# Optimization experiments

Measured on AMD Instinct MI355X. Metric: run time of the kernel, lower is better.

## Reference

```python
import jax, jax.numpy as jnp
import numpy as np

T, H, I, E, K = 4096, 2048, 1408, 8, 2  # tokens, hidden, intermediate, experts, top_k


def setup_inputs() -> dict:
    key = jax.random.key(0)
    ks = jax.random.split(key, 6)
    hidden_states = jax.random.normal(ks[0], (T, H), dtype=jnp.float32)
    gate_weight = jax.random.normal(ks[1], (E, H), dtype=jnp.float32) * 0.02  # fp32 gate, per source assert
    w13_weight = jax.random.randint(ks[2], (E, 2 * I, H), -127, 128, dtype=jnp.int8)
    w13_weight_scale = jax.random.uniform(ks[3], (E, 2 * I), dtype=jnp.float32, minval=0.5, maxval=1.5) * 0.005
    w2_weight = jax.random.randint(ks[4], (E, H, I), -127, 128, dtype=jnp.int8)
    w2_weight_scale = jax.random.uniform(ks[5], (E, H), dtype=jnp.float32, minval=0.5, maxval=1.5) * 0.005
    return dict(hidden_states=hidden_states, gate_weight=gate_weight,
                w13_weight=w13_weight, w13_weight_scale=w13_weight_scale,
                w2_weight=w2_weight, w2_weight_scale=w2_weight_scale)


def _dynamic_quant_i8(x):
    # per-token dynamic symmetric int8: scale = max|x|/127 (smooth scales default to ones)
    s = jnp.maximum(jnp.max(jnp.abs(x), axis=-1, keepdims=True) / 127.0, 1e-8)
    q = jnp.clip(jnp.round(x / s), -127.0, 127.0)
    return q, s


def reference(hidden_states, gate_weight, w13_weight, w13_weight_scale, w2_weight, w2_weight_scale):
    # --- gating: fp32 linear + topk softmax (renormalize=True) ---
    logits = hidden_states @ gate_weight.T              # [T, E]
    probs = jax.nn.softmax(logits, axis=-1)
    topv, topi = jax.lax.top_k(probs, K)                # [T, K]
    gates = topv / jnp.sum(topv, axis=-1, keepdims=True)
    # dense routing weights [T, E]: gate value where expert selected, else 0
    route = jnp.zeros((T, E), hidden_states.dtype).at[jnp.arange(T)[:, None], topi].add(gates)

    # --- dynamic per-token int8 quant of routed input (same token value for each of its K copies) ---
    q_in, s_in = _dynamic_quant_i8(hidden_states)       # [T, H], [T, 1]

    # --- grouped w8a8 GEMM (fc1) -> SwiGLU -> requant -> grouped GEMM (fc2) -> weighted combine ---
    def step(acc, xs):
        w13, s13, w2, s2w, r = xs                       # per-expert weights / route column [T]
        h1 = (q_in @ w13.T.astype(jnp.float32)) * s_in * s13[None, :]   # dequant fc1: [T, 2I]
        g, u = h1[:, :I], h1[:, I:]
        act = jax.nn.silu(g) * u                        # SwiGLU
        q_a, s_a = _dynamic_quant_i8(act)
        h2 = (q_a @ w2.T.astype(jnp.float32)) * s_a * s2w[None, :]      # dequant fc2: [T, H]
        return acc + r[:, None] * h2, None

    acc0 = jnp.zeros_like(hidden_states)
    out, _ = jax.lax.scan(step, acc0,
                          (w13_weight, w13_weight_scale, w2_weight, w2_weight_scale, route.T))
    return out
```

## Files before the change

kernel.cpp:

```cpp
#include <hip/hip_runtime.h>
#include <hip/hip_bf16.h>

#define T_TOK 4096
#define H_DIM 2048
#define I_DIM 1408
#define E_NUM 8
#define NI2   (2 * I_DIM)
#define NMB   136

typedef int v4i __attribute__((ext_vector_type(4)));

#define GLD_LDS16(gptr, lptr)                                                        \
  __builtin_amdgcn_global_load_lds(                                                  \
      (const __attribute__((address_space(1))) void*)(gptr),                         \
      (__attribute__((address_space(3))) void*)(lptr), 16, 0, 0)

__global__ __launch_bounds__(256) void pack_tiled(
    const int* __restrict__ w13, const int* __restrict__ w2,
    signed char* __restrict__ qw13t, signed char* __restrict__ qw2t) {
  const int id = blockIdx.x;
  const int* src;
  signed char* dst;
  int R, Kd, nb, kc, e;
  if (id < 8 * 22 * 32) {
    e = id / (22 * 32);
    int r = id % (22 * 32);
    nb = r / 32; kc = r % 32;
    src = w13; dst = qw13t + (size_t)id * 8192; R = NI2; Kd = H_DIM;
  } else {
    int j = id - 8 * 22 * 32;
    e = j / (16 * 22);
    int r = j % (16 * 22);
    nb = r / 22; kc = r % 22;
    src = w2; dst = qw2t + (size_t)j * 8192; R = H_DIM; Kd = I_DIM;
  }
  const int tid = threadIdx.x;
  const int seg = tid & 3;
#pragma unroll
  for (int h = 0; h < 2; h++) {
    int row = h * 64 + (tid >> 2);
    const int4* s4 = (const int4*)(src + ((size_t)(e * R + nb * 128 + row) * Kd + kc * 64 + seg * 16));
    int4 v0 = s4[0], v1 = s4[1], v2 = s4[2], v3 = s4[3];
    union { signed char c[16]; int4 v; } pk;
    pk.c[0] = (signed char)v0.x;  pk.c[1] = (signed char)v0.y;
    pk.c[2] = (signed char)v0.z;  pk.c[3] = (signed char)v0.w;
    pk.c[4] = (signed char)v1.x;  pk.c[5] = (signed char)v1.y;
    pk.c[6] = (signed char)v1.z;  pk.c[7] = (signed char)v1.w;
    pk.c[8] = (signed char)v2.x;  pk.c[9] = (signed char)v2.y;
    pk.c[10] = (signed char)v2.z; pk.c[11] = (signed char)v2.w;
    pk.c[12] = (signed char)v3.x; pk.c[13] = (signed char)v3.y;
    pk.c[14] = (signed char)v3.z; pk.c[15] = (signed char)v3.w;
    *(int4*)(dst + h * 4096 + tid * 16) = pk.v;
  }
}

__global__ __launch_bounds__(256) void gate_route_quant(
    const float* __restrict__ hs, const float* __restrict__ gw,
    signed char* __restrict__ qin, float* __restrict__ s_in,
    int* __restrict__ tope, float* __restrict__ gts) {
  const int t = blockIdx.x;
  const int tid = threadIdx.x;
  const int lane = tid & 63;
  const int wave = tid >> 6;
  const float* row = hs + (size_t)t * H_DIM;

  const float4* r4 = (const float4*)row + tid * 2;
  float4 xa = r4[0], xb = r4[1];
  float x[8] = {xa.x, xa.y, xa.z, xa.w, xb.x, xb.y, xb.z, xb.w};

  double pd[8];
  for (int e = 0; e < 8; e++) pd[e] = 0.0;
  float am = 0.f;
  for (int j = 0; j < 8; j++) {
    float v = x[j];
    am = fmaxf(am, fabsf(v));
    int col = tid * 8 + j;
    for (int e = 0; e < 8; e++)
      pd[e] += (double)v * (double)gw[e * H_DIM + col];
  }
  for (int e = 0; e < 8; e++)
    for (int s = 32; s; s >>= 1) pd[e] += __shfl_down(pd[e], s);
  for (int s = 32; s; s >>= 1) am = fmaxf(am, __shfl_down(am, s));

  __shared__ double sred[4][8];
  __shared__ float sam[4];
  __shared__ float sbc;
  if (lane == 0) {
    for (int e = 0; e < 8; e++) sred[wave][e] = pd[e];
    sam[wave] = am;
  }
  __syncthreads();
  if (tid == 0) {
    float l[8];
    for (int e = 0; e < 8; e++)
      l[e] = (float)(sred[0][e] + sred[1][e] + sred[2][e] + sred[3][e]);
    float amx = fmaxf(fmaxf(sam[0], sam[1]), fmaxf(sam[2], sam[3]));
    float s = fmaxf(amx / 127.0f, 1e-8f);
    s_in[t] = s;
    sbc = s;
    int i1 = 0;
    for (int e = 1; e < 8; e++) if (l[e] > l[i1]) i1 = e;
    int i2 = -1;
    for (int e = 0; e < 8; e++) {
      if (e == i1) continue;
      if (i2 < 0 || l[e] > l[i2]) i2 = e;
    }
    float d = expf(l[i2] - l[i1]);
    tope[2 * t] = i1;     gts[2 * t] = 1.0f / (1.0f + d);
    tope[2 * t + 1] = i2; gts[2 * t + 1] = d / (1.0f + d);
  }
  __syncthreads();
  float s = sbc;
  union { signed char c[8]; unsigned long long u; } pk;
  for (int j = 0; j < 8; j++) {
    float q = rintf(x[j] / s);
    q = fminf(127.f, fmaxf(-127.f, q));
    pk.c[j] = (signed char)q;
  }
  ((unsigned long long*)(qin + (size_t)t * H_DIM))[tid] = pk.u;
}

__global__ __launch_bounds__(256) void build_lists(
    const int* __restrict__ tope, int* __restrict__ tok_list,
    int* __restrict__ epos, int* __restrict__ cnt) {
  const int e = blockIdx.x;
  const int tid = threadIdx.x;
  const int lane = tid & 63;
  const int wave = tid >> 6;
  __shared__ int wsum[4];
  __shared__ int base_s;
  if (tid == 0) base_s = 0;
  __syncthreads();
  for (int t0 = 0; t0 < T_TOK; t0 += 256) {
    int t = t0 + tid;
    int i1 = tope[2 * t], i2 = tope[2 * t + 1];
    int slot = (i1 == e) ? 0 : ((i2 == e) ? 1 : -1);
    unsigned long long m = __ballot(slot >= 0);
    int wpre = __popcll(m & ((1ull << lane) - 1ull));
    if (lane == 0) wsum[wave] = __popcll(m);
    __syncthreads();
    int pre = wpre;
    for (int w = 0; w < wave; w++) pre += wsum[w];
    int total = wsum[0] + wsum[1] + wsum[2] + wsum[3];
    int b = base_s;
    if (slot >= 0) {
      int pos = b + pre;
      tok_list[e * T_TOK + pos] = t;
      epos[2 * t + slot] = (e << 16) | pos;
    }
    __syncthreads();
    if (tid == 0) base_s = b + total;
  }
  __syncthreads();
  if (tid == 0) cnt[e] = base_s;
}

__global__ void calc_off(const int* __restrict__ cnt, int* __restrict__ poff) {
  if (threadIdx.x == 0) {
    int p = 0;
    for (int e = 0; e < E_NUM; e++) {
      poff[e] = p;
      p += ((cnt[e] + 63) >> 6) << 6;
    }
  }
}

__global__ __launch_bounds__(256) void tile_a1(
    const signed char* __restrict__ qin, const int* __restrict__ tok_list,
    const int* __restrict__ cnt, const int* __restrict__ poff,
    signed char* __restrict__ qx1) {
  const int e = blockIdx.y;
  const int ce = cnt[e];
  const int m0 = blockIdx.x * 64;
  if (m0 >= ce) return;
  const int pmb = (poff[e] >> 6) + blockIdx.x;
  const int tid = threadIdx.x;
  const int row = tid >> 2, seg = tid & 3;
  const int tok = tok_list[e * T_TOK + min(m0 + row, ce - 1)];
  const signed char* src = qin + (size_t)tok * H_DIM + seg * 16;
  signed char* dstb = qx1 + (size_t)pmb * (32 * 4096) + tid * 16;
#pragma unroll
  for (int kc = 0; kc < 32; kc++)
    *(int4*)(dstb + kc * 4096) = *(const int4*)(src + kc * 64);
}

__global__ __launch_bounds__(256, 3) void gemm1_silu(
    const signed char* __restrict__ qw13t, const signed char* __restrict__ qx1,
    const float* __restrict__ s_in, const float* __restrict__ s13,
    const int* __restrict__ tok_list, const int* __restrict__ cnt,
    const int* __restrict__ poff, __hip_bfloat16* __restrict__ act,
    unsigned int* __restrict__ amax) {
  const int xcd = blockIdx.x & 7;
  const int r = blockIdx.x >> 3;
  const int sl = r >> 6;
  const int mb = r & 63;
  const int s = xcd + 8 * sl;
  const int e = s / 11;
  const int nb = s % 11;

  const int ce = cnt[e];
  const int m0 = mb * 64;
  if (m0 >= ce) return;
  const int n0 = nb * 128;
  const int pmb = (poff[e] >> 6) + mb;

  __shared__ __align__(16) signed char As[4096];
  __shared__ __align__(16) signed char Bg[8192];
  __shared__ __align__(16) signed char Bu[8192];

  const int tid = threadIdx.x;
  const int lane = tid & 63;
  const int wave = tid >> 6;
  const int quad = lane >> 4;
  const int ln = lane & 15;

  const signed char* Ab = qx1 + (size_t)pmb * (32 * 4096) + tid * 16;
  const signed char* Bgb = qw13t + (size_t)(e * 22 + nb) * 32 * 8192 + tid * 16;
  const signed char* Bub = qw13t + (size_t)(e * 22 + nb + 11) * 32 * 8192 + tid * 16;
  const int ldsu = (tid & ~63) * 16;

  v4i accg[4][2], accu[4][2];
  v4i zero = {0, 0, 0, 0};
#pragma unroll
  for (int i = 0; i < 4; i++)
#pragma unroll
    for (int j = 0; j < 2; j++) { accg[i][j] = zero; accu[i][j] = zero; }

  for (int kc = 0; kc < 32; kc++) {
    __syncthreads();
    GLD_LDS16(Ab + (size_t)kc * 4096, As + ldsu);
    GLD_LDS16(Bgb + (size_t)kc * 8192, Bg + ldsu);
    GLD_LDS16(Bgb + (size_t)kc * 8192 + 4096, Bg + 4096 + ldsu);
    GLD_LDS16(Bub + (size_t)kc * 8192, Bu + ldsu);
    GLD_LDS16(Bub + (size_t)kc * 8192 + 4096, Bu + 4096 + ldsu);
    __syncthreads();

    v4i af[4], bgf[2], buf_[2];
#pragma unroll
    for (int mt = 0; mt < 4; mt++)
      af[mt] = *(const v4i*)(As + (mt * 16 + ln) * 64 + quad * 16);
#pragma unroll
    for (int nt = 0; nt < 2; nt++) {
      bgf[nt] = *(const v4i*)(Bg + (wave * 32 + nt * 16 + ln) * 64 + quad * 16);
      buf_[nt] = *(const v4i*)(Bu + (wave * 32 + nt * 16 + ln) * 64 + quad * 16);
    }
#pragma unroll
    for (int mt = 0; mt < 4; mt++)
#pragma unroll
      for (int nt = 0; nt < 2; nt++) {
        accg[mt][nt] = __builtin_amdgcn_mfma_i32_16x16x64_i8(af[mt], bgf[nt], accg[mt][nt], 0, 0, 0);
        accu[mt][nt] = __builtin_amdgcn_mfma_i32_16x16x64_i8(af[mt], buf_[nt], accu[mt][nt], 0, 0, 0);
      }
  }

  const float* s13e = s13 + e * NI2;
  float sg[2], su[2];
  int ncol[2];
#pragma unroll
  for (int nt = 0; nt < 2; nt++) {
    int n = n0 + wave * 32 + nt * 16 + ln;
    ncol[nt] = n;
    sg[nt] = s13e[n];
    su[nt] = s13e[I_DIM + n];
  }
  const int* tl = tok_list + e * T_TOK;
  const int pbase = poff[e];
#pragma unroll
  for (int mt = 0; mt < 4; mt++) {
#pragma unroll
    for (int r2 = 0; r2 < 4; r2++) {
      int mrel = m0 + mt * 16 + quad * 4 + r2;
      bool valid = mrel < ce;
      int tok = tl[valid ? mrel : 0];
      float si = s_in[tok];
      size_t prow = (size_t)(pbase + mrel);
      __hip_bfloat16* arow = act + prow * I_DIM;
      float am = 0.f;
#pragma unroll
      for (int nt = 0; nt < 2; nt++) {
        float g = (float)accg[mt][nt][r2] * si * sg[nt];
        float u = (float)accu[mt][nt][r2] * si * su[nt];
        float a = g / (1.0f + expf(-g)) * u;
        if (valid) arow[ncol[nt]] = __float2bfloat16(a);
        am = fmaxf(am, fabsf(a));
      }
      for (int sh = 1; sh < 16; sh <<= 1) am = fmaxf(am, __shfl_xor(am, sh, 16));
      if (valid && ln == 0) atomicMax(amax + prow, __float_as_uint(am));
    }
  }
}

__global__ __launch_bounds__(256) void quant_act(
    const __hip_bfloat16* __restrict__ act, const unsigned int* __restrict__ amax,
    const int* __restrict__ cnt, const int* __restrict__ poff,
    signed char* __restrict__ qx2, float* __restrict__ s_a) {
  const int e = blockIdx.y;
  const int ce = cnt[e];
  const int m0 = blockIdx.x * 64;
  if (m0 >= ce) return;
  const int pmb = (poff[e] >> 6) + blockIdx.x;
  const int tid = threadIdx.x;
  const int row = tid >> 2, seg = tid & 3;
  const int mrel = m0 + row;
  const bool valid = mrel < ce;
  const size_t prow = (size_t)poff[e] + mrel;
  float s = fmaxf(__uint_as_float(amax[prow]) / 127.0f, 1e-8f);
  if (valid && seg == 0) s_a[prow] = s;
  const unsigned short* arow = (const unsigned short*)(act + prow * I_DIM) + seg * 16;
  signed char* dstb = qx2 + (size_t)pmb * (22 * 4096) + tid * 16;
  for (int kc = 0; kc < 22; kc++) {
    union { int4 v[2]; unsigned short u[16]; } in;
    union { signed char c[16]; int4 v; } pk;
    if (valid) {
      in.v[0] = *(const int4*)(arow + kc * 64);
      in.v[1] = *(const int4*)(arow + kc * 64 + 8);
#pragma unroll
      for (int j = 0; j < 16; j++) {
        float f = __uint_as_float((unsigned)in.u[j] << 16);
        float q = rintf(f / s);
        q = fminf(127.f, fmaxf(-127.f, q));
        pk.c[j] = (signed char)q;
      }
    } else {
      pk.v = int4{0, 0, 0, 0};
    }
    *(int4*)(dstb + kc * 4096) = pk.v;
  }
}

__global__ __launch_bounds__(256, 4) void gemm2_h2(
    const signed char* __restrict__ qw2t, const signed char* __restrict__ qx2,
    const float* __restrict__ s_a, const float* __restrict__ s2w,
    const int* __restrict__ cnt, const int* __restrict__ poff,
    float* __restrict__ h2s) {
  const int xcd = blockIdx.x & 7;
  const int r = blockIdx.x >> 3;
  const int sl = r >> 6;
  const int mb = r & 63;
  const int s = xcd + 8 * sl;
  const int e = s >> 4;
  const int nb = s & 15;

  const int ce = cnt[e];
  const int m0 = mb * 64;
  if (m0 >= ce) return;
  const int n0 = nb * 128;
  const int pmb = (poff[e] >> 6) + mb;

  __shared__ __align__(16) signed char As[4096];
  __shared__ __align__(16) signed char Bs[8192];

  const int tid = threadIdx.x;
  const int lane = tid & 63;
  const int wave = tid >> 6;
  const int quad = lane >> 4;
  const int ln = lane & 15;

  const signed char* Ab = qx2 + (size_t)pmb * (22 * 4096) + tid * 16;
  const signed char* Bb = qw2t + (size_t)(e * 16 + nb) * 22 * 8192 + tid * 16;
  const int ldsu = (tid & ~63) * 16;

  v4i acc[4][2];
  v4i zero = {0, 0, 0, 0};
#pragma unroll
  for (int i = 0; i < 4; i++)
#pragma unroll
    for (int j = 0; j < 2; j++) acc[i][j] = zero;

  for (int kc = 0; kc < 22; kc++) {
    __syncthreads();
    GLD_LDS16(Ab + (size_t)kc * 4096, As + ldsu);
    GLD_LDS16(Bb + (size_t)kc * 8192, Bs + ldsu);
    GLD_LDS16(Bb + (size_t)kc * 8192 + 4096, Bs + 4096 + ldsu);
    __syncthreads();

    v4i af[4], bf[2];
#pragma unroll
    for (int mt = 0; mt < 4; mt++)
      af[mt] = *(const v4i*)(As + (mt * 16 + ln) * 64 + quad * 16);
#pragma unroll
    for (int nt = 0; nt < 2; nt++)
      bf[nt] = *(const v4i*)(Bs + (wave * 32 + nt * 16 + ln) * 64 + quad * 16);
#pragma unroll
    for (int mt = 0; mt < 4; mt++)
#pragma unroll
      for (int nt = 0; nt < 2; nt++)
        acc[mt][nt] = __builtin_amdgcn_mfma_i32_16x16x64_i8(af[mt], bf[nt], acc[mt][nt], 0, 0, 0);
  }

  const float* s2e = s2w + e * H_DIM;
  float sw[2];
  int ncol[2];
#pragma unroll
  for (int nt = 0; nt < 2; nt++) {
    int n = n0 + wave * 32 + nt * 16 + ln;
    ncol[nt] = n;
    sw[nt] = s2e[n];
  }
  const int pbase = poff[e];
#pragma unroll
  for (int mt = 0; mt < 4; mt++) {
#pragma unroll
    for (int r2 = 0; r2 < 4; r2++) {
      int mrel = m0 + mt * 16 + quad * 4 + r2;
      if (mrel >= ce) continue;
      size_t prow = (size_t)(pbase + mrel);
      float sa = s_a[prow];
      float* orow = h2s + prow * H_DIM;
#pragma unroll
      for (int nt = 0; nt < 2; nt++)
        orow[ncol[nt]] = (float)acc[mt][nt][r2] * sa * sw[nt];
    }
  }
}

__global__ __launch_bounds__(256) void gather_out(
    const float* __restrict__ h2s, const int* __restrict__ epos,
    const float* __restrict__ gts, const int* __restrict__ poff,
    float* __restrict__ out) {
  const int t = blockIdx.x;
  int a = epos[2 * t], b = epos[2 * t + 1];
  float g1 = gts[2 * t], g2 = gts[2 * t + 1];
  int r1 = poff[a >> 16] + (a & 0xffff);
  int r2 = poff[b >> 16] + (b & 0xffff);
  const float4* R1 = (const float4*)(h2s + (size_t)r1 * H_DIM);
  const float4* R2 = (const float4*)(h2s + (size_t)r2 * H_DIM);
  float4* O = (float4*)(out + (size_t)t * H_DIM);
  for (int c = threadIdx.x; c < H_DIM / 4; c += 256) {
    float4 x = R1[c], y = R2[c];
    float4 z;
    z.x = g1 * x.x + g2 * y.x;
    z.y = g1 * x.y + g2 * y.y;
    z.z = g1 * x.z + g2 * y.z;
    z.w = g1 * x.w + g2 * y.w;
    O[c] = z;
  }
}

extern "C" void kernel_launch(void* const* d_in, const int* in_sizes, int n_in,
                              void* d_out, int out_size, void* d_ws, size_t ws_size,
                              hipStream_t stream) {
  const float* hs = (const float*)d_in[0];
  const float* gw = (const float*)d_in[1];
  const int* w13 = (const int*)d_in[2];
  const float* s13 = (const float*)d_in[3];
  const int* w2 = (const int*)d_in[4];
  const float* s2w = (const float*)d_in[5];
  float* out = (float*)d_out;

  const int PR = NMB * 64;

  char* ws = (char*)d_ws;
  size_t o = 0;
  auto take = [&](size_t b) {
    char* p = ws + o;
    o += (b + 255) & ~(size_t)255;
    return p;
  };
  signed char* qw13t = (signed char*)take((size_t)E_NUM * NI2 * H_DIM);
  signed char* qin = (signed char*)take((size_t)T_TOK * H_DIM);
  signed char* qx1 = (signed char*)take((size_t)PR * H_DIM);
  float* h2s = (float*)qw13t;
  __hip_bfloat16* act = (__hip_bfloat16*)take((size_t)PR * I_DIM * 2);
  signed char* qw2t = (signed char*)take((size_t)E_NUM * H_DIM * I_DIM);
  signed char* qx2 = (signed char*)take((size_t)PR * I_DIM);
  float* sin_ = (float*)take((size_t)T_TOK * 4);
  float* sa = (float*)take((size_t)PR * 4);
  unsigned int* amax = (unsigned int*)take((size_t)PR * 4);
  int* tokl = (int*)take((size_t)E_NUM * T_TOK * 4);
  int* tope = (int*)take((size_t)T_TOK * 2 * 4);
  int* epos = (int*)take((size_t)T_TOK * 2 * 4);
  float* gts = (float*)take((size_t)T_TOK * 2 * 4);
  int* cnt = (int*)take(E_NUM * 4);
  int* poff = (int*)take(E_NUM * 4);

  hipMemsetAsync(amax, 0, (size_t)PR * 4, stream);

  pack_tiled<<<8 * 22 * 32 + 8 * 16 * 22, 256, 0, stream>>>(w13, w2, qw13t, qw2t);
  gate_route_quant<<<T_TOK, 256, 0, stream>>>(hs, gw, qin, sin_, tope, gts);
  build_lists<<<E_NUM, 256, 0, stream>>>(tope, tokl, epos, cnt);
  calc_off<<<1, 64, 0, stream>>>(cnt, poff);
  {
    dim3 g(64, 8);
    tile_a1<<<g, 256, 0, stream>>>(qin, tokl, cnt, poff, qx1);
  }
  gemm1_silu<<<8 * 11 * 64, 256, 0, stream>>>(qw13t, qx1, sin_, s13, tokl, cnt, poff, act, amax);
  {
    dim3 g(64, 8);
    quant_act<<<g, 256, 0, stream>>>(act, amax, cnt, poff, qx2, sa);
  }
  gemm2_h2<<<8 * 16 * 64, 256, 0, stream>>>(qw2t, qx2, sa, s2w, cnt, poff, h2s);
  gather_out<<<T_TOK, 256, 0, stream>>>(h2s, epos, gts, poff, out);
}
```

Baseline: 606.5 us.

## Double-buffer LDS tiles in both grouped int8 GEMM kernels

Both the fc1 (gate/up) and fc2 grouped GEMM kernels now keep two LDS buffers per operand. The next K-chunk is prefetched with global_load_lds before the MFMAs on the current chunk run, and the loop uses one barrier per iteration instead of two. The aim is to hide global-load latency behind matrix math. In exchange, LDS use per block doubles, which may lower occupancy. The compiler may also insert conservative vmcnt waits before the LDS reads, which would remove the overlap.

```diff
diff --git a/kernel.cpp b/kernel.cpp
--- a/kernel.cpp
+++ b/kernel.cpp
@@ -204,9 +204,9 @@
   const int n0 = nb * 128;
   const int pmb = (poff[e] >> 6) + mb;
 
-  __shared__ __align__(16) signed char As[4096];
-  __shared__ __align__(16) signed char Bg[8192];
-  __shared__ __align__(16) signed char Bu[8192];
+  __shared__ __align__(16) signed char As[2][4096];
+  __shared__ __align__(16) signed char Bg[2][8192];
+  __shared__ __align__(16) signed char Bu[2][8192];
 
   const int tid = threadIdx.x;
   const int lane = tid & 63;
@@ -219,6 +219,14 @@
   const signed char* Bub = qw13t + (size_t)(e * 22 + nb + 11) * 32 * 8192 + tid * 16;
   const int ldsu = (tid & ~63) * 16;
 
+  auto stage = [&](int kc, int b) {
+    GLD_LDS16(Ab + (size_t)kc * 4096, As[b] + ldsu);
+    GLD_LDS16(Bgb + (size_t)kc * 8192, Bg[b] + ldsu);
+    GLD_LDS16(Bgb + (size_t)kc * 8192 + 4096, Bg[b] + 4096 + ldsu);
+    GLD_LDS16(Bub + (size_t)kc * 8192, Bu[b] + ldsu);
+    GLD_LDS16(Bub + (size_t)kc * 8192 + 4096, Bu[b] + 4096 + ldsu);
+  };
+
   v4i accg[4][2], accu[4][2];
   v4i zero = {0, 0, 0, 0};
 #pragma unroll
@@ -226,23 +234,20 @@
 #pragma unroll
     for (int j = 0; j < 2; j++) { accg[i][j] = zero; accu[i][j] = zero; }
 
+  stage(0, 0);
   for (int kc = 0; kc < 32; kc++) {
     __syncthreads();
-    GLD_LDS16(Ab + (size_t)kc * 4096, As + ldsu);
-    GLD_LDS16(Bgb + (size_t)kc * 8192, Bg + ldsu);
-    GLD_LDS16(Bgb + (size_t)kc * 8192 + 4096, Bg + 4096 + ldsu);
-    GLD_LDS16(Bub + (size_t)kc * 8192, Bu + ldsu);
-    GLD_LDS16(Bub + (size_t)kc * 8192 + 4096, Bu + 4096 + ldsu);
-    __syncthreads();
+    if (kc + 1 < 32) stage(kc + 1, (kc + 1) & 1);
+    const int b = kc & 1;
 
     v4i af[4], bgf[2], buf_[2];
 #pragma unroll
     for (int mt = 0; mt < 4; mt++)
-      af[mt] = *(const v4i*)(As + (mt * 16 + ln) * 64 + quad * 16);
+      af[mt] = *(const v4i*)(As[b] + (mt * 16 + ln) * 64 + quad * 16);
 #pragma unroll
     for (int nt = 0; nt < 2; nt++) {
-      bgf[nt] = *(const v4i*)(Bg + (wave * 32 + nt * 16 + ln) * 64 + quad * 16);
-      buf_[nt] = *(const v4i*)(Bu + (wave * 32 + nt * 16 + ln) * 64 + quad * 16);
+      bgf[nt] = *(const v4i*)(Bg[b] + (wave * 32 + nt * 16 + ln) * 64 + quad * 16);
+      buf_[nt] = *(const v4i*)(Bu[b] + (wave * 32 + nt * 16 + ln) * 64 + quad * 16);
     }
 #pragma unroll
     for (int mt = 0; mt < 4; mt++)
@@ -347,8 +352,8 @@
   const int n0 = nb * 128;
   const int pmb = (poff[e] >> 6) + mb;
 
-  __shared__ __align__(16) signed char As[4096];
-  __shared__ __align__(16) signed char Bs[8192];
+  __shared__ __align__(16) signed char As[2][4096];
+  __shared__ __align__(16) signed char Bs[2][8192];
 
   const int tid = threadIdx.x;
   const int lane = tid & 63;
@@ -360,6 +365,12 @@
   const signed char* Bb = qw2t + (size_t)(e * 16 + nb) * 22 * 8192 + tid * 16;
   const int ldsu = (tid & ~63) * 16;
 
+  auto stage = [&](int kc, int b) {
+    GLD_LDS16(Ab + (size_t)kc * 4096, As[b] + ldsu);
+    GLD_LDS16(Bb + (size_t)kc * 8192, Bs[b] + ldsu);
+    GLD_LDS16(Bb + (size_t)kc * 8192 + 4096, Bs[b] + 4096 + ldsu);
+  };
+
   v4i acc[4][2];
   v4i zero = {0, 0, 0, 0};
 #pragma unroll
@@ -367,20 +378,19 @@
 #pragma unroll
     for (int j = 0; j < 2; j++) acc[i][j] = zero;
 
+  stage(0, 0);
   for (int kc = 0; kc < 22; kc++) {
     __syncthreads();
-    GLD_LDS16(Ab + (size_t)kc * 4096, As + ldsu);
-    GLD_LDS16(Bb + (size_t)kc * 8192, Bs + ldsu);
-    GLD_LDS16(Bb + (size_t)kc * 8192 + 4096, Bs + 4096 + ldsu);
-    __syncthreads();
+    if (kc + 1 < 22) stage(kc + 1, (kc + 1) & 1);
+    const int b = kc & 1;
 
     v4i af[4], bf[2];
 #pragma unroll
     for (int mt = 0; mt < 4; mt++)
-      af[mt] = *(const v4i*)(As + (mt * 16 + ln) * 64 + quad * 16);
+      af[mt] = *(const v4i*)(As[b] + (mt * 16 + ln) * 64 + quad * 16);
 #pragma unroll
     for (int nt = 0; nt < 2; nt++)
-      bf[nt] = *(const v4i*)(Bs + (wave * 32 + nt * 16 + ln) * 64 + quad * 16);
+      bf[nt] = *(const v4i*)(Bs[b] + (wave * 32 + nt * 16 + ln) * 64 + quad * 16);
 #pragma unroll
     for (int mt = 0; mt < 4; mt++)
 #pragma unroll
```

Result: slower. 618.8 us (+2.0%).
